# Optimization experiments

Hardware: AMD Instinct MI355X
Metric: run time of the kernel (lower is better)

The kernel has to match this reference:

```python
import jax, jax.numpy as jnp
import numpy as np

S, B, D = 2048, 1, 4096
H, HKV, DH = 32, 8, 128
THETA = 10000.0


def _rope_tables(seq_len, dim, theta):
    inv_freq = 1.0 / (theta ** (jnp.arange(0, dim, 2, dtype=jnp.float32) / dim))
    freqs = jnp.arange(seq_len, dtype=jnp.float32)[:, None] * inv_freq[None, :]  # [S, DH/2]
    return jnp.cos(freqs), jnp.sin(freqs)


def _apply_rope(x, cos, sin):
    # x: [B, H, S, DH]; non-interleaved (flash_attn interleaved=False) rotation
    half = x.shape[-1] // 2
    x1, x2 = x[..., :half], x[..., half:]
    c = cos[None, None, :, :]
    s = sin[None, None, :, :]
    return jnp.concatenate([x1 * c - x2 * s, x2 * c + x1 * s], axis=-1)


def setup_inputs() -> dict:
    key = jax.random.key(0)
    k1, k2, k3 = jax.random.split(key, 3)
    hidden_states = jax.random.normal(k1, (S, B, D), dtype=jnp.float32)
    W_qkv = jax.random.normal(k2, (D, (H + 2 * HKV) * DH), dtype=jnp.float32) * 0.02
    W_o = jax.random.normal(k3, (H * DH, D), dtype=jnp.float32) * 0.02
    sequence_mask = jnp.ones((B, S), dtype=jnp.int32)
    return {"hidden_states": hidden_states, "sequence_mask": sequence_mask,
            "W_qkv": W_qkv, "W_o": W_o}


def reference(hidden_states, sequence_mask, W_qkv, W_o):
    s, b, _ = hidden_states.shape
    qkv = hidden_states @ W_qkv  # [S, B, (H+2*HKV)*DH]
    q, k, v = jnp.split(qkv, [H * DH, H * DH + HKV * DH], axis=-1)
    q = q.reshape(s, b, H, DH).transpose(1, 2, 0, 3)    # [B, H, S, DH]
    k = k.reshape(s, b, HKV, DH).transpose(1, 2, 0, 3)  # [B, HKV, S, DH]
    v = v.reshape(s, b, HKV, DH).transpose(1, 2, 0, 3)

    cos, sin = _rope_tables(s, DH, THETA)
    q = _apply_rope(q, cos, sin)
    k = _apply_rope(k, cos, sin)

    # GQA: repeat kv heads
    rep = H // HKV
    k = jnp.repeat(k, rep, axis=1)  # [B, H, S, DH]
    v = jnp.repeat(v, rep, axis=1)

    scale = 1.0 / jnp.sqrt(jnp.asarray(DH, dtype=q.dtype))
    scores = jnp.einsum('bhqd,bhkd->bhqk', q, k) * scale
    causal = jnp.tril(jnp.ones((s, s), dtype=bool))
    scores = jnp.where(causal[None, None, :, :], scores, jnp.finfo(scores.dtype).min)
    attn = jax.nn.softmax(scores, axis=-1)
    ctx = jnp.einsum('bhqk,bhkd->bhqd', attn, v)  # [B, H, S, DH]
    ctx = ctx.transpose(2, 0, 1, 3).reshape(s, b, H * DH)  # [S, B, H*DH]
    out = ctx @ W_o  # [S, B, D]
    return out
```

## Files before the change

kernel.cpp:

```cpp
#include <hip/hip_runtime.h>

typedef unsigned short u16;
typedef __bf16 bf16x8 __attribute__((ext_vector_type(8)));
typedef float f32x4 __attribute__((ext_vector_type(4)));
typedef u16 u16x4 __attribute__((ext_vector_type(4)));

constexpr int SEQ = 2048;
constexpr int NQKV = 6144;

__device__ __forceinline__ float bf2f(u16 x) {
    unsigned int u = ((unsigned int)x) << 16;
    return __builtin_bit_cast(float, u);
}
__device__ __forceinline__ u16 f2bf(float f) {
    unsigned int u = __builtin_bit_cast(unsigned int, f);
    u += 0x7FFF + ((u >> 16) & 1);
    return (u16)(u >> 16);
}

__device__ __forceinline__ void gload16(const void* g, void* l) {
    void* gg = const_cast<void*>(g);
    __builtin_amdgcn_global_load_lds(
        (__attribute__((address_space(1))) void*)gg,
        (__attribute__((address_space(3))) void*)l, 16, 0, 0);
}

__device__ __forceinline__ void gatebar(int G) {
    if (G == 8) asm volatile("s_waitcnt vmcnt(8)" ::: "memory");
    else if (G == 4) asm volatile("s_waitcnt vmcnt(4)" ::: "memory");
    else asm volatile("s_waitcnt vmcnt(0)" ::: "memory");
    __builtin_amdgcn_sched_barrier(0);
    __builtin_amdgcn_s_barrier();
    __builtin_amdgcn_sched_barrier(0);
}

__global__ void rope_table_k(float* __restrict__ tab) {
    int idx = blockIdx.x * 256 + threadIdx.x;
    if (idx >= SEQ * 64) return;
    int s = idx >> 6;
    int i = idx & 63;
    float invf = expf(-(float)i * (float)(1.0 / 64.0) * logf(10000.0f));
    float ang = (float)s * invf;
    float sv, cv;
    sincosf(ang, &sv, &cv);
    tab[idx * 2] = cv;
    tab[idx * 2 + 1] = sv;
}

__global__ __launch_bounds__(256) void cast_k(const float* __restrict__ src,
                                              u16* __restrict__ dst, int n4) {
    int i = blockIdx.x * 256 + threadIdx.x;
    if (i >= n4) return;
    f32x4 v = *(const f32x4*)&src[(size_t)i * 4];
    u16x4 o;
#pragma unroll
    for (int j = 0; j < 4; ++j) o[j] = f2bf(v[j]);
    *(u16x4*)&dst[(size_t)i * 4] = o;
}

__global__ __launch_bounds__(256) void transpose_cast_k(const float* __restrict__ src,
                                                        u16* __restrict__ dst, int R, int C) {
    __shared__ u16 tile[64][65];
    int t = threadIdx.x;
    int bx = blockIdx.x, by = blockIdx.y;
    int r0 = by * 64, c0 = bx * 64;
#pragma unroll
    for (int it = 0; it < 4; ++it) {
        int row = it * 16 + (t >> 4);
        int col = (t & 15) * 4;
        f32x4 v = *(const f32x4*)&src[(size_t)(r0 + row) * C + c0 + col];
        tile[row][col] = f2bf(v[0]); tile[row][col + 1] = f2bf(v[1]);
        tile[row][col + 2] = f2bf(v[2]); tile[row][col + 3] = f2bf(v[3]);
    }
    __syncthreads();
#pragma unroll
    for (int it = 0; it < 4; ++it) {
        int orow = it * 16 + (t >> 4);
        int ocol = (t & 15) * 4;
        u16x4 v;
        v[0] = tile[ocol][orow]; v[1] = tile[ocol + 1][orow];
        v[2] = tile[ocol + 2][orow]; v[3] = tile[ocol + 3][orow];
        *(u16x4*)&dst[(size_t)(c0 + orow) * R + r0 + ocol] = v;
    }
}

__global__ __launch_bounds__(256) void transpose_vt_k(const u16* __restrict__ QKV,
                                                      u16* __restrict__ VTg) {
    __shared__ u16 tile[64][65];
    int t = threadIdx.x;
    int s0 = blockIdx.x * 64;
    int hv = blockIdx.y >> 1;
    int d0 = (blockIdx.y & 1) * 64;
    const u16* src = QKV + (size_t)s0 * NQKV + 5120 + hv * 128 + d0;
#pragma unroll
    for (int it = 0; it < 4; ++it) {
        int row = it * 16 + (t >> 4);
        int col = (t & 15) * 4;
        u16x4 v = *(const u16x4*)&src[(size_t)row * NQKV + col];
        tile[row][col] = v[0]; tile[row][col + 1] = v[1];
        tile[row][col + 2] = v[2]; tile[row][col + 3] = v[3];
    }
    __syncthreads();
    u16* dst = VTg + (size_t)hv * 128 * SEQ + (size_t)d0 * SEQ + s0;
#pragma unroll
    for (int it = 0; it < 4; ++it) {
        int orow = it * 16 + (t >> 4);
        int ocol = (t & 15) * 4;
        u16x4 v;
        v[0] = tile[ocol][orow]; v[1] = tile[ocol + 1][orow];
        v[2] = tile[ocol + 2][orow]; v[3] = tile[ocol + 3][orow];
        *(u16x4*)&dst[(size_t)orow * SEQ + ocol] = v;
    }
}

__global__ __launch_bounds__(512, 2) void gemm1_big_k(const u16* __restrict__ A,
                                                      const u16* __restrict__ BT,
                                                      u16* __restrict__ C) {
    constexpr int K = 4096, N = 6144;
    constexpr int SBUF = 57344;
    __shared__ alignas(16) char lds[2 * SBUF];

    int t = threadIdx.x;
    int lane = t & 63, w = t >> 6;
    int wr = w >> 1, wc = w & 1;
    int l15 = lane & 15, l4 = lane >> 4;

    int wg = blockIdx.x;
    int xcd = wg & 7, j = wg >> 3;
    int bm = ((xcd >> 2) << 2) + (j >> 3);
    int bn = ((xcd & 3) << 3) + (j & 7);

    const u16* Ab = A + (size_t)bm * 256 * K;
    const u16* Bb = BT + (size_t)bn * 192 * K;

    const u16* ga[4]; int da[4];
#pragma unroll
    for (int i = 0; i < 4; ++i) {
        int c = t + i * 512;
        int row = c >> 3;
        int ch = (c & 7) ^ (row & 7);
        ga[i] = Ab + (size_t)row * K + ch * 8;
        da[i] = c * 16;
    }
    const u16* gb[3]; int db[3];
#pragma unroll
    for (int i = 0; i < 3; ++i) {
        int c = t + i * 512;
        int row = c >> 3;
        int ch = (c & 7) ^ (row & 7);
        gb[i] = Bb + (size_t)row * K + ch * 8;
        db[i] = 32768 + c * 16;
    }

    auto stage = [&](int kt) {
        char* L = lds + (kt & 1) * SBUF;
        int ko = kt * 64;
#pragma unroll
        for (int i = 0; i < 4; ++i) gload16(ga[i] + ko, L + da[i]);
#pragma unroll
        for (int i = 0; i < 3; ++i) gload16(gb[i] + ko, L + db[i]);
    };

    f32x4 acc[4][6];
#pragma unroll
    for (int i = 0; i < 4; ++i)
#pragma unroll
        for (int j2 = 0; j2 < 6; ++j2) acc[i][j2] = f32x4{0.f, 0.f, 0.f, 0.f};

    int arow[4];
#pragma unroll
    for (int fm = 0; fm < 4; ++fm) arow[fm] = wr * 64 + fm * 16 + l15;
    int brow[6];
#pragma unroll
    for (int fn = 0; fn < 6; ++fn) brow[fn] = wc * 96 + fn * 16 + l15;

    stage(0);
    gatebar(0);

    for (int kt = 0; kt < 64; ++kt) {
        const u16* L = (const u16*)(lds + (kt & 1) * SBUF);
        if (kt + 1 < 64) stage(kt + 1);
        bf16x8 bf[6][2];
#pragma unroll
        for (int fn = 0; fn < 6; ++fn)
#pragma unroll
            for (int kk = 0; kk < 2; ++kk) {
                int ch = (kk * 4 + l4) ^ (brow[fn] & 7);
                bf[fn][kk] = *(const bf16x8*)&L[16384 + brow[fn] * 64 + ch * 8];
            }
#pragma unroll
        for (int p = 0; p < 2; ++p) {
            bf16x8 af[2][2];
#pragma unroll
            for (int f2 = 0; f2 < 2; ++f2)
#pragma unroll
                for (int kk = 0; kk < 2; ++kk) {
                    int r = arow[p * 2 + f2];
                    int ch = (kk * 4 + l4) ^ (r & 7);
                    af[f2][kk] = *(const bf16x8*)&L[r * 64 + ch * 8];
                }
            __builtin_amdgcn_s_setprio(1);
#pragma unroll
            for (int f2 = 0; f2 < 2; ++f2)
#pragma unroll
                for (int kk = 0; kk < 2; ++kk)
#pragma unroll
                    for (int fn = 0; fn < 6; ++fn)
                        acc[p * 2 + f2][fn] = __builtin_amdgcn_mfma_f32_16x16x32_bf16(
                            af[f2][kk], bf[fn][kk], acc[p * 2 + f2][fn], 0, 0, 0);
            __builtin_amdgcn_s_setprio(0);
        }
        gatebar(0);
    }

#pragma unroll
    for (int fm = 0; fm < 4; ++fm)
#pragma unroll
        for (int fn = 0; fn < 6; ++fn)
#pragma unroll
            for (int i = 0; i < 4; ++i) {
                int row = bm * 256 + wr * 64 + fm * 16 + l4 * 4 + i;
                int col = bn * 192 + wc * 96 + fn * 16 + l15;
                C[(size_t)row * N + col] = f2bf(acc[fm][fn][i]);
            }
}

__global__ __launch_bounds__(512, 2) void gemm2_big_k(const u16* __restrict__ A,
                                                      const u16* __restrict__ BT,
                                                      float* __restrict__ C) {
    constexpr int K = 4096, N = 4096;
    constexpr int SBUF = 49152;
    __shared__ alignas(16) char lds[2 * SBUF];

    int t = threadIdx.x;
    int lane = t & 63, w = t >> 6;
    int wr = w >> 1, wc = w & 1;
    int l15 = lane & 15, l4 = lane >> 4;

    int wg = blockIdx.x;
    int xcd = wg & 7, j = wg >> 3;
    int bm = ((xcd >> 2) << 2) + (j >> 3);
    int bn = ((xcd & 3) << 3) + (j & 7);

    const u16* Ab = A + (size_t)bm * 256 * K;
    const u16* Bb = BT + (size_t)bn * 128 * K;

    const u16* ga[4]; int da[4];
#pragma unroll
    for (int i = 0; i < 4; ++i) {
        int c = t + i * 512;
        int row = c >> 3;
        int ch = (c & 7) ^ (row & 7);
        ga[i] = Ab + (size_t)row * K + ch * 8;
        da[i] = c * 16;
    }
    const u16* gb[2]; int db[2];
#pragma unroll
    for (int i = 0; i < 2; ++i) {
        int c = t + i * 512;
        int row = c >> 3;
        int ch = (c & 7) ^ (row & 7);
        gb[i] = Bb + (size_t)row * K + ch * 8;
        db[i] = 32768 + c * 16;
    }

    auto stage = [&](int kt) {
        char* L = lds + (kt & 1) * SBUF;
        int ko = kt * 64;
#pragma unroll
        for (int i = 0; i < 4; ++i) gload16(ga[i] + ko, L + da[i]);
#pragma unroll
        for (int i = 0; i < 2; ++i) gload16(gb[i] + ko, L + db[i]);
    };

    f32x4 acc[4][4];
#pragma unroll
    for (int i = 0; i < 4; ++i)
#pragma unroll
        for (int j2 = 0; j2 < 4; ++j2) acc[i][j2] = f32x4{0.f, 0.f, 0.f, 0.f};

    int arow[4];
#pragma unroll
    for (int fm = 0; fm < 4; ++fm) arow[fm] = wr * 64 + fm * 16 + l15;
    int brow[4];
#pragma unroll
    for (int fn = 0; fn < 4; ++fn) brow[fn] = wc * 64 + fn * 16 + l15;

    stage(0);
    gatebar(0);

    for (int kt = 0; kt < 64; ++kt) {
        const u16* L = (const u16*)(lds + (kt & 1) * SBUF);
        if (kt + 1 < 64) stage(kt + 1);
        bf16x8 bf[4][2];
#pragma unroll
        for (int fn = 0; fn < 4; ++fn)
#pragma unroll
            for (int kk = 0; kk < 2; ++kk) {
                int ch = (kk * 4 + l4) ^ (brow[fn] & 7);
                bf[fn][kk] = *(const bf16x8*)&L[16384 + brow[fn] * 64 + ch * 8];
            }
#pragma unroll
        for (int p = 0; p < 2; ++p) {
            bf16x8 af[2][2];
#pragma unroll
            for (int f2 = 0; f2 < 2; ++f2)
#pragma unroll
                for (int kk = 0; kk < 2; ++kk) {
                    int r = arow[p * 2 + f2];
                    int ch = (kk * 4 + l4) ^ (r & 7);
                    af[f2][kk] = *(const bf16x8*)&L[r * 64 + ch * 8];
                }
            __builtin_amdgcn_s_setprio(1);
#pragma unroll
            for (int f2 = 0; f2 < 2; ++f2)
#pragma unroll
                for (int kk = 0; kk < 2; ++kk)
#pragma unroll
                    for (int fn = 0; fn < 4; ++fn)
                        acc[p * 2 + f2][fn] = __builtin_amdgcn_mfma_f32_16x16x32_bf16(
                            af[f2][kk], bf[fn][kk], acc[p * 2 + f2][fn], 0, 0, 0);
            __builtin_amdgcn_s_setprio(0);
        }
        gatebar(0);
    }

#pragma unroll
    for (int fm = 0; fm < 4; ++fm)
#pragma unroll
        for (int fn = 0; fn < 4; ++fn)
#pragma unroll
            for (int i = 0; i < 4; ++i) {
                int row = bm * 256 + wr * 64 + fm * 16 + l4 * 4 + i;
                int col = bn * 128 + wc * 64 + fn * 16 + l15;
                C[(size_t)row * N + col] = acc[fm][fn][i];
            }
}

__global__ __launch_bounds__(256) void repack_rope_k(const u16* __restrict__ QKV,
                                                     const float* __restrict__ tab,
                                                     u16* __restrict__ Ko) {
    int idx = blockIdx.x * 256 + threadIdx.x;
    int i4 = (idx & 15) * 4;
    int su = idx >> 4;
    int u = su & 7;
    int s = su >> 3;
    const float* tp = tab + (s * 64 + i4) * 2;
    f32x4 t0 = *(const f32x4*)tp;
    f32x4 t1 = *(const f32x4*)(tp + 4);
    float cv[4] = {t0[0], t0[2], t1[0], t1[2]};
    float sv[4] = {t0[1], t0[3], t1[1], t1[3]};
    const u16* base = QKV + (size_t)s * NQKV + 4096 + u * 128;
    u16* ob = Ko + ((size_t)u * SEQ + s) * 128;
    u16x4 x1 = *(const u16x4*)(base + i4);
    u16x4 x2 = *(const u16x4*)(base + 64 + i4);
    u16x4 o1, o2;
#pragma unroll
    for (int j = 0; j < 4; ++j) {
        float a = bf2f(x1[j]), b = bf2f(x2[j]);
        o1[j] = f2bf(a * cv[j] - b * sv[j]);
        o2[j] = f2bf(b * cv[j] + a * sv[j]);
    }
    *(u16x4*)(ob + i4) = o1;
    *(u16x4*)(ob + 64 + i4) = o2;
}

__global__ __launch_bounds__(512) void attn_k(const u16* __restrict__ QKVg,
                                              const u16* __restrict__ Kg,
                                              const u16* __restrict__ VTg,
                                              const float* __restrict__ tab,
                                              u16* __restrict__ ctx) {
    constexpr float SCL2 = 0.08838834764831845f * 1.44269504088896340736f;
    constexpr float THR = 11.5f;
    __shared__ alignas(16) u16 Klds[2][128 * 128];
    __shared__ alignas(16) u16 VTl[2][128 * 128];
    __shared__ alignas(16) u16 Plds[8 * 16 * 72];

    int t = threadIdx.x;
    int lane = t & 63, w = t >> 6;
    int l15 = lane & 15, l4 = lane >> 4;
    int bx = blockIdx.x;
    int h = blockIdx.y, hkv = h >> 2;
    const u16* Kh = Kg + (size_t)hkv * SEQ * 128;
    const u16* Vh = VTg + (size_t)hkv * 128 * SEQ;
    u16* Pw = &Plds[w * 1152];

    int kr[4], kchs[4];
#pragma unroll
    for (int i2 = 0; i2 < 4; ++i2) {
        int c = t + i2 * 512;
        kr[i2] = c >> 4;
        kchs[i2] = (c & 15) ^ (kr[i2] & 7);
    }
    int vd[4], vchs[4];
#pragma unroll
    for (int i2 = 0; i2 < 4; ++i2) {
        int c = t + i2 * 512;
        vd[i2] = c >> 4;
        vchs[i2] = (c & 15) ^ (vd[i2] & 7);
    }

    int q0 = bx * 128;
    int ntA = bx + 1;

    bf16x8 qf[4];
    f32x4 o[8];
    float m_i[4], l_i[4];

    auto kvbase = [&](int tt) { return (tt < ntA ? tt : tt - ntA) << 7; };
    auto load_q = [&]() {
        int s = q0 + w * 16 + l15;
        const u16* Qh = QKVg + (size_t)s * NQKV + h * 128;
        bf16x8 raw[4];
#pragma unroll
        for (int ks = 0; ks < 4; ++ks) raw[ks] = *(const bf16x8*)(Qh + ks * 32 + l4 * 8);
        const float* tp0 = tab + ((size_t)s * 64 + l4 * 8) * 2;
        const float* tp1 = tp0 + 64;
        float c0[8], s0[8], c1[8], s1[8];
#pragma unroll
        for (int v4 = 0; v4 < 4; ++v4) {
            f32x4 a = *(const f32x4*)(tp0 + v4 * 4);
            c0[v4 * 2] = a[0]; s0[v4 * 2] = a[1];
            c0[v4 * 2 + 1] = a[2]; s0[v4 * 2 + 1] = a[3];
            f32x4 b2 = *(const f32x4*)(tp1 + v4 * 4);
            c1[v4 * 2] = b2[0]; s1[v4 * 2] = b2[1];
            c1[v4 * 2 + 1] = b2[2]; s1[v4 * 2 + 1] = b2[3];
        }
        const u16* r0 = (const u16*)&raw[0];
        const u16* r1 = (const u16*)&raw[1];
        const u16* r2 = (const u16*)&raw[2];
        const u16* r3 = (const u16*)&raw[3];
        u16* q0p = (u16*)&qf[0];
        u16* q1p = (u16*)&qf[1];
        u16* q2p = (u16*)&qf[2];
        u16* q3p = (u16*)&qf[3];
#pragma unroll
        for (int j = 0; j < 8; ++j) {
            float x0 = bf2f(r0[j]), x1 = bf2f(r1[j]);
            float x2 = bf2f(r2[j]), x3 = bf2f(r3[j]);
            q0p[j] = f2bf(x0 * c0[j] - x2 * s0[j]);
            q2p[j] = f2bf(x2 * c0[j] + x0 * s0[j]);
            q1p[j] = f2bf(x1 * c1[j] - x3 * s1[j]);
            q3p[j] = f2bf(x3 * c1[j] + x1 * s1[j]);
        }
    };
    auto reset_acc = [&]() {
#pragma unroll
        for (int nf = 0; nf < 8; ++nf) o[nf] = f32x4{0.f, 0.f, 0.f, 0.f};
#pragma unroll
        for (int i = 0; i < 4; ++i) { m_i[i] = -3.0e38f; l_i[i] = 0.f; }
    };
    auto write_ctx = [&]() {
        float inv[4];
#pragma unroll
        for (int i = 0; i < 4; ++i) {
            float rs = l_i[i];
            rs += __shfl_xor(rs, 1);
            rs += __shfl_xor(rs, 2);
            rs += __shfl_xor(rs, 4);
            rs += __shfl_xor(rs, 8);
            inv[i] = 1.0f / rs;
        }
#pragma unroll
        for (int nf = 0; nf < 8; ++nf)
#pragma unroll
            for (int i = 0; i < 4; ++i) {
                int qrow = q0 + w * 16 + l4 * 4 + i;
                ctx[(size_t)qrow * 4096 + h * 128 + nf * 16 + l15] = f2bf(o[nf][i] * inv[i]);
            }
    };
    auto stage = [&](int tt) {
        int kv0 = kvbase(tt);
        const u16* Kt = Kh + (size_t)kv0 * 128;
        char* kb = (char*)Klds[tt & 1];
        char* vb = (char*)VTl[tt & 1];
#pragma unroll
        for (int i2 = 0; i2 < 4; ++i2)
            gload16(Kt + kr[i2] * 128 + kchs[i2] * 8, kb + (size_t)(t + i2 * 512) * 16);
#pragma unroll
        for (int i2 = 0; i2 < 4; ++i2)
            gload16(Vh + (size_t)vd[i2] * SEQ + kv0 + vchs[i2] * 8,
                    vb + (size_t)(t + i2 * 512) * 16);
    };

    load_q();
    reset_acc();
    stage(0);

    for (int tt = 0; tt < 17; ++tt) {
        __builtin_amdgcn_s_barrier();
        __builtin_amdgcn_sched_barrier(0);
        bool nxt = (tt + 1 < 17);
        if (nxt) stage(tt + 1);
        gatebar(nxt ? 8 : 0);
        if (tt == ntA) {
            write_ctx();
            q0 = (15 - bx) * 128;
            load_q();
            reset_acc();
        }

        int b = tt & 1;
        int kv0 = kvbase(tt);
        const u16* KL = Klds[b];
        const u16* VL = VTl[b];

        f32x4 sa[8];
#pragma unroll
        for (int cg = 0; cg < 8; ++cg) {
            sa[cg] = f32x4{0.f, 0.f, 0.f, 0.f};
            int row = cg * 16 + l15;
#pragma unroll
            for (int ks = 0; ks < 4; ++ks) {
                int chs = (ks * 4 + l4) ^ (row & 7);
                bf16x8 kf = *(const bf16x8*)&KL[row * 128 + chs * 8];
                sa[cg] = __builtin_amdgcn_mfma_f32_16x16x32_bf16(qf[ks], kf, sa[cg], 0, 0, 0);
            }
        }
#pragma unroll
        for (int cg = 0; cg < 8; ++cg)
#pragma unroll
            for (int i = 0; i < 4; ++i) sa[cg][i] *= SCL2;
        if (kv0 + 127 > q0 + w * 16) {
#pragma unroll
            for (int cg = 0; cg < 8; ++cg) {
                int col = kv0 + cg * 16 + l15;
#pragma unroll
                for (int i = 0; i < 4; ++i) {
                    int qrow = q0 + w * 16 + l4 * 4 + i;
                    if (col > qrow) sa[cg][i] = -3.0e38f;
                }
            }
        }
        float lmx[4];
#pragma unroll
        for (int i = 0; i < 4; ++i) {
            float a0 = fmaxf(fmaxf(sa[0][i], sa[1][i]), fmaxf(sa[2][i], sa[3][i]));
            float a1 = fmaxf(fmaxf(sa[4][i], sa[5][i]), fmaxf(sa[6][i], sa[7][i]));
            lmx[i] = fmaxf(a0, a1);
        }
        bool defer = __all((lmx[0] <= m_i[0] + THR) & (lmx[1] <= m_i[1] + THR) &
                           (lmx[2] <= m_i[2] + THR) & (lmx[3] <= m_i[3] + THR));
        if (!defer) {
            float corr[4];
#pragma unroll
            for (int i = 0; i < 4; ++i) {
                float m0 = lmx[i];
                m0 = fmaxf(m0, __shfl_xor(m0, 1));
                m0 = fmaxf(m0, __shfl_xor(m0, 2));
                m0 = fmaxf(m0, __shfl_xor(m0, 4));
                m0 = fmaxf(m0, __shfl_xor(m0, 8));
                float mnew = fmaxf(m_i[i], m0);
                corr[i] = __builtin_amdgcn_exp2f(m_i[i] - mnew);
                m_i[i] = mnew;
                l_i[i] *= corr[i];
            }
#pragma unroll
            for (int nf = 0; nf < 8; ++nf) {
                o[nf][0] *= corr[0]; o[nf][1] *= corr[1];
                o[nf][2] *= corr[2]; o[nf][3] *= corr[3];
            }
        }
#pragma unroll
        for (int hf = 0; hf < 2; ++hf) {
#pragma unroll
            for (int i = 0; i < 4; ++i) {
                int prow = l4 * 4 + i;
                int sw = (prow >> 1) & 3;
                float rs = 0.f;
#pragma unroll
                for (int cg = 0; cg < 4; ++cg) {
                    float p = __builtin_amdgcn_exp2f(sa[hf * 4 + cg][i] - m_i[i]);
                    rs += p;
                    int ch = cg * 2 + (l15 >> 3);
                    Pw[prow * 72 + ((ch ^ sw) << 3) + (l15 & 7)] = f2bf(p);
                }
                l_i[i] += rs;
            }
            asm volatile("s_waitcnt lgkmcnt(0)" ::: "memory");
            __builtin_amdgcn_sched_barrier(0);
#pragma unroll
            for (int kst = 0; kst < 2; ++kst) {
                int pchs = (kst * 4 + l4) ^ ((l15 >> 1) & 3);
                bf16x8 pf = *(const bf16x8*)&Pw[l15 * 72 + pchs * 8];
                int kst2 = hf * 2 + kst;
#pragma unroll
                for (int nf = 0; nf < 8; ++nf) {
                    int d = nf * 16 + l15;
                    int vch = (kst2 * 4 + l4) ^ (d & 7);
                    bf16x8 vf = *(const bf16x8*)&VL[d * 128 + vch * 8];
                    o[nf] = __builtin_amdgcn_mfma_f32_16x16x32_bf16(pf, vf, o[nf], 0, 0, 0);
                }
            }
        }
    }
    write_ctx();
}

extern "C" void kernel_launch(void* const* d_in, const int* in_sizes, int n_in,
                              void* d_out, int out_size, void* d_ws, size_t ws_size,
                              hipStream_t stream) {
    const float* hidden = (const float*)d_in[0];
    const float* Wqkv = (const float*)d_in[2];
    const float* Wo = (const float*)d_in[3];
    float* out = (float*)d_out;
    char* ws = (char*)d_ws;

    u16* QKV     = (u16*)(ws + 0);
    u16* WqkvT   = (u16*)(ws + 25165824);
    u16* Kb      = (u16*)(ws + 25165824);
    u16* VTg     = (u16*)(ws + 29360128);
    float* tab   = (float*)(ws + 33554432);
    u16* WoT     = (u16*)(ws + 34603008);
    u16* ctx     = (u16*)(ws + 68157440);
    u16* hiddenB = (u16*)(ws + 75497472);

    cast_k<<<8192, 256, 0, stream>>>(hidden, hiddenB, 2048 * 4096 / 4);
    transpose_cast_k<<<dim3(96, 64), 256, 0, stream>>>(Wqkv, WqkvT, 4096, 6144);
    gemm1_big_k<<<256, 512, 0, stream>>>(hiddenB, WqkvT, QKV);
    rope_table_k<<<512, 256, 0, stream>>>(tab);
    repack_rope_k<<<1024, 256, 0, stream>>>(QKV, tab, Kb);
    transpose_vt_k<<<dim3(32, 16), 256, 0, stream>>>(QKV, VTg);
    transpose_cast_k<<<dim3(64, 64), 256, 0, stream>>>(Wo, WoT, 4096, 4096);
    attn_k<<<dim3(8, 32), 512, 0, stream>>>(QKV, Kb, VTg, tab, ctx);
    gemm2_big_k<<<256, 512, 0, stream>>>(ctx, WoT, out);
}
```

Measured before the change: 296.8 us.

## Triple-buffer output-projection GEMM loads and fold softmax scale into Q

The output-projection GEMM moves from double to triple LDS buffering, prefetching two k-tiles ahead and waiting only on the oldest tile's loads (vmcnt(6)) instead of draining all loads every iteration. Separately, the attention kernel now applies the softmax scale to Q once during RoPE rather than scaling every score tile. The triple buffer raises LDS use to 144 KB per block, which likely makes the launch_bounds(512,2) occupancy target unreachable. Scaling Q before bf16 rounding also changes numerics slightly.

```diff
diff --git a/kernel.cpp b/kernel.cpp
--- a/kernel.cpp
+++ b/kernel.cpp
@@ -27,6 +27,7 @@
 
 __device__ __forceinline__ void gatebar(int G) {
     if (G == 8) asm volatile("s_waitcnt vmcnt(8)" ::: "memory");
+    else if (G == 6) asm volatile("s_waitcnt vmcnt(6)" ::: "memory");
     else if (G == 4) asm volatile("s_waitcnt vmcnt(4)" ::: "memory");
     else asm volatile("s_waitcnt vmcnt(0)" ::: "memory");
     __builtin_amdgcn_sched_barrier(0);
@@ -230,7 +231,7 @@
                                                       float* __restrict__ C) {
     constexpr int K = 4096, N = 4096;
     constexpr int SBUF = 49152;
-    __shared__ alignas(16) char lds[2 * SBUF];
+    __shared__ alignas(16) char lds[3 * SBUF];
 
     int t = threadIdx.x;
     int lane = t & 63, w = t >> 6;
@@ -264,8 +265,8 @@
         db[i] = 32768 + c * 16;
     }
 
-    auto stage = [&](int kt) {
-        char* L = lds + (kt & 1) * SBUF;
+    auto stage = [&](int kt, int b) {
+        char* L = lds + b * SBUF;
         int ko = kt * 64;
 #pragma unroll
         for (int i = 0; i < 4; ++i) gload16(ga[i] + ko, L + da[i]);
@@ -286,12 +287,16 @@
 #pragma unroll
     for (int fn = 0; fn < 4; ++fn) brow[fn] = wc * 64 + fn * 16 + l15;
 
-    stage(0);
-    gatebar(0);
-
+    stage(0, 0);
+    stage(1, 1);
+    gatebar(6);
+
+    int b = 0;
+    int b2 = 2;
     for (int kt = 0; kt < 64; ++kt) {
-        const u16* L = (const u16*)(lds + (kt & 1) * SBUF);
-        if (kt + 1 < 64) stage(kt + 1);
+        const u16* L = (const u16*)(lds + b * SBUF);
+        bool pf = (kt + 2 < 64);
+        if (pf) stage(kt + 2, b2);
         bf16x8 bf[4][2];
 #pragma unroll
         for (int fn = 0; fn < 4; ++fn)
@@ -322,7 +327,9 @@
                             af[f2][kk], bf[fn][kk], acc[p * 2 + f2][fn], 0, 0, 0);
             __builtin_amdgcn_s_setprio(0);
         }
-        gatebar(0);
+        if (kt < 63) gatebar(pf ? 6 : 0);
+        b = (b == 2) ? 0 : b + 1;
+        b2 = (b2 == 2) ? 0 : b2 + 1;
     }
 
 #pragma unroll
@@ -438,10 +445,10 @@
         for (int j = 0; j < 8; ++j) {
             float x0 = bf2f(r0[j]), x1 = bf2f(r1[j]);
             float x2 = bf2f(r2[j]), x3 = bf2f(r3[j]);
-            q0p[j] = f2bf(x0 * c0[j] - x2 * s0[j]);
-            q2p[j] = f2bf(x2 * c0[j] + x0 * s0[j]);
-            q1p[j] = f2bf(x1 * c1[j] - x3 * s1[j]);
-            q3p[j] = f2bf(x3 * c1[j] + x1 * s1[j]);
+            q0p[j] = f2bf((x0 * c0[j] - x2 * s0[j]) * SCL2);
+            q2p[j] = f2bf((x2 * c0[j] + x0 * s0[j]) * SCL2);
+            q1p[j] = f2bf((x1 * c1[j] - x3 * s1[j]) * SCL2);
+            q3p[j] = f2bf((x3 * c1[j] + x1 * s1[j]) * SCL2);
         }
     };
     auto reset_acc = [&]() {
@@ -517,10 +524,6 @@
                 sa[cg] = __builtin_amdgcn_mfma_f32_16x16x32_bf16(qf[ks], kf, sa[cg], 0, 0, 0);
             }
         }
-#pragma unroll
-        for (int cg = 0; cg < 8; ++cg)
-#pragma unroll
-            for (int i = 0; i < 4; ++i) sa[cg][i] *= SCL2;
         if (kv0 + 127 > q0 + w * 16) {
 #pragma unroll
             for (int cg = 0; cg < 8; ++cg) {
```

After: 293.5 us. About the same (-1.1%).
